# Kernel optimization log

Hardware: AMD Instinct MI355X
Metric: run time of the kernel (lower is better)

The kernel has to match this reference:

```python
import jax, jax.numpy as jnp
import numpy as np

B, T, C, HR = 8, 4096, 256, 4
N_LAYER, LAYER_ID = 12, 3
HID = HR * C


def _fancy_decay_first():
    # Faithful reproduction of VRWKV_SpatialMix._init_weights(init_mode='fancy')
    r01 = LAYER_ID / (N_LAYER - 1)
    h = np.arange(C, dtype=np.float32)
    decay = -5.0 + 8.0 * (h / (C - 1)) ** (0.7 + 1.3 * r01)
    zig = ((np.arange(1, C + 1) % 3) - 1).astype(np.float32) * 0.5
    first = np.float32(np.log(0.3)) + zig
    return jnp.asarray(decay, jnp.float32), jnp.asarray(first, jnp.float32)


def setup_inputs() -> dict:
    key = jax.random.key(0)
    ks = jax.random.split(key, 12)
    s = 0.02  # small weight scale keeps exp(k) well-conditioned
    decay, first = _fancy_decay_first()
    return {
        "x": jax.random.normal(ks[0], (B, T, C), jnp.float32),
        "Wk": jax.random.normal(ks[1], (C, C), jnp.float32) * s,
        "Wv": jax.random.normal(ks[2], (C, C), jnp.float32) * s,
        "Wr": jax.random.normal(ks[3], (C, C), jnp.float32) * s,
        "Wo": jax.random.normal(ks[4], (C, C), jnp.float32) * s,
        "Wk_ffn": jax.random.normal(ks[5], (C, HID), jnp.float32) * s,
        "Wv_ffn": jax.random.normal(ks[6], (HID, C), jnp.float32) * s,
        "Wr_ffn": jax.random.normal(ks[7], (C, C), jnp.float32) * s,
        "g1": 1.0 + 0.1 * jax.random.normal(ks[8], (C,), jnp.float32),
        "b1": 0.1 * jax.random.normal(ks[9], (C,), jnp.float32),
        "g2": 1.0 + 0.1 * jax.random.normal(ks[10], (C,), jnp.float32),
        "b2": 0.1 * jax.random.normal(ks[11], (C,), jnp.float32),
        "spatial_decay": decay,
        "spatial_first": first,
    }


def _ln(x, g, b):
    m = jnp.mean(x, axis=-1, keepdims=True)
    v = jnp.var(x, axis=-1, keepdims=True)
    return (x - m) * jax.lax.rsqrt(v + 1e-5) * g + b


def _wkv(w, u, k, v):
    # Numerically-stable log-space WKV recurrence (same math as wkv_cuda):
    # y_t = (sum_{i<t} e^{w*(t-1-i)+k_i} v_i + e^{u+k_t} v_t)
    #     / (sum_{i<t} e^{w*(t-1-i)+k_i}     + e^{u+k_t})
    # w,u: [C]; k,v: [B,T,C] -> y: [B,T,C]
    Bb, Tt, Cc = k.shape
    kT = jnp.swapaxes(k, 0, 1)  # [T,B,C]
    vT = jnp.swapaxes(v, 0, 1)

    def step(carry, kv):
        p, q, o = carry           # [B,C] num / den / running max exponent
        kt, vt = kv               # [B,C]
        no = jnp.maximum(o, u + kt)
        A = jnp.exp(o - no)
        E = jnp.exp(u + kt - no)
        y = (A * p + E * vt) / (A * q + E)
        no2 = jnp.maximum(w + o, kt)
        A2 = jnp.exp(w + o - no2)
        E2 = jnp.exp(kt - no2)
        return (A2 * p + E2 * vt, A2 * q + E2, no2), y

    init = (jnp.zeros((Bb, Cc), k.dtype),
            jnp.zeros((Bb, Cc), k.dtype),
            jnp.full((Bb, Cc), -1e38, k.dtype))
    _, yT = jax.lax.scan(step, init, (kT, vT))
    return jnp.swapaxes(yT, 0, 1)


def reference(x, Wk, Wv, Wr, Wo, Wk_ffn, Wv_ffn, Wr_ffn, g1, b1, g2, b2,
              spatial_decay, spatial_first):
    Tlen = x.shape[1]
    # --- SpatialMix (shift_pixel=0 -> xk=xv=xr=h, key_norm=False) ---
    h = _ln(x, g1, b1)
    k = h @ Wk
    v = h @ Wv
    sr = jax.nn.sigmoid(h @ Wr)
    y = _wkv(spatial_decay / Tlen, spatial_first / Tlen, k, v)
    x = x + (sr * y) @ Wo
    # --- ChannelMix (square-ReLU MLP, sigmoid receptance gate) ---
    h2 = _ln(x, g2, b2)
    kk = jnp.square(jax.nn.relu(h2 @ Wk_ffn))
    x = x + jax.nn.sigmoid(h2 @ Wr_ffn) * (kk @ Wv_ffn)
    return x
```

## Files before the change

kernel.cpp:

```cpp
#include <hip/hip_runtime.h>
#include <hip/hip_bf16.h>
#include <math.h>

#define TDIM 4096
#define CDIM 256
#define BDIM 8
#define NTOK (BDIM * TDIM)
#define HIDDIM 1024
#define NCHUNK 256
#define CHLEN 16
#define NSEG 8
#define SEGCH 32

typedef float f32x4 __attribute__((ext_vector_type(4)));
typedef __bf16 bf16x8 __attribute__((ext_vector_type(8)));
typedef __bf16 bf16x4 __attribute__((ext_vector_type(4)));
typedef long long i64x2 __attribute__((ext_vector_type(2)));

#define GLDS16(gp, lp) __builtin_amdgcn_global_load_lds( \
    (const __attribute__((address_space(1))) void*)(gp), \
    (__attribute__((address_space(3))) void*)(lp), 16, 0, 0)

#define WAITCNT_VM8  0x0F78
#define WAITCNT_VM5  0x0F75
#define WAITCNT_VM4  0x0F74
#define WAITCNT_VM2  0x0F72
#define WAITCNT_VM0  0x0F70
#define WAITCNT_LGKM0 0xC07F

#define STAGE_FENCE() do { \
    __builtin_amdgcn_sched_barrier(0); \
    __builtin_amdgcn_s_waitcnt(WAITCNT_LGKM0); \
    __builtin_amdgcn_s_barrier(); \
    __builtin_amdgcn_sched_barrier(0); \
  } while (0)

__device__ __forceinline__ float sigm(float v) { return 1.0f / (1.0f + __expf(-v)); }

__device__ __forceinline__ int permk(int k) {
  return (k & ~63) + (((k >> 3) & 3) << 4) + (((k >> 5) & 1) << 3) + (k & 7);
}

__global__ __launch_bounds__(256) void prep(
    const float* __restrict__ Wk, const float* __restrict__ Wv,
    const float* __restrict__ Wr, const float* __restrict__ Wo,
    const float* __restrict__ Wkf, const float* __restrict__ Wvf,
    const float* __restrict__ Wrf,
    __bf16* __restrict__ WoT, unsigned char* __restrict__ Wkvr8,
    unsigned char* __restrict__ Wkfr8, unsigned char* __restrict__ Wvf8,
    const float* __restrict__ x, const float* __restrict__ gamma,
    const float* __restrict__ beta, unsigned char* __restrict__ h8) {
  if (blockIdx.x >= 1024) {
    const int wave = threadIdx.x >> 6, lane = threadIdx.x & 63;
    const long long row = (long long)(blockIdx.x - 1024) * 4 + wave;
    const long long base = row * CDIM + lane * 4;
    const f32x4 v = *(const f32x4*)&x[base];
    float s = v[0] + v[1] + v[2] + v[3];
    float s2 = v[0]*v[0] + v[1]*v[1] + v[2]*v[2] + v[3]*v[3];
    #pragma unroll
    for (int o = 1; o < 64; o <<= 1) { s += __shfl_xor(s, o); s2 += __shfl_xor(s2, o); }
    const float mean = s * (1.0f / CDIM);
    const float var = s2 * (1.0f / CDIM) - mean * mean;
    const float rstd = rsqrtf(var + 1e-5f);
    const f32x4 g4 = *(const f32x4*)&gamma[lane * 4];
    const f32x4 b4 = *(const f32x4*)&beta[lane * 4];
    float o0 = (v[0] - mean) * rstd * g4[0] + b4[0];
    float o1 = (v[1] - mean) * rstd * g4[1] + b4[1];
    float o2 = (v[2] - mean) * rstd * g4[2] + b4[2];
    float o3 = (v[3] - mean) * rstd * g4[3] + b4[3];
    int w = 0;
    w = __builtin_amdgcn_cvt_pk_fp8_f32(o0, o1, w, false);
    w = __builtin_amdgcn_cvt_pk_fp8_f32(o2, o3, w, true);
    *(int*)&h8[row * CDIM + permk(lane * 4)] = w;
    return;
  }
  long long j = (long long)blockIdx.x * 256 + threadIdx.x;
  if (j < 49152) {
    const long long d = j * 4;
    const int n = (int)(d >> 8), k0 = (int)(d & 255);
    const float* src = (n < 256) ? Wk : (n < 512 ? Wv : Wr);
    const int nn = n & 255;
    int w = 0;
    w = __builtin_amdgcn_cvt_pk_fp8_f32(src[k0 * 256 + nn],
                                        src[(k0 + 1) * 256 + nn], w, false);
    w = __builtin_amdgcn_cvt_pk_fp8_f32(src[(k0 + 2) * 256 + nn],
                                        src[(k0 + 3) * 256 + nn], w, true);
    *(int*)&Wkvr8[(long long)n * 256 + permk(k0)] = w;
    return;
  }
  j -= 49152;
  if (j < 65536) { int n = (int)(j >> 8), k = (int)(j & 255);
    WoT[j] = (__bf16)Wo[k * 256 + n]; return; }
  j -= 65536;
  if (j < 81920) {
    const long long d = j * 4;
    const int n = (int)(d >> 8), k0 = (int)(d & 255);
    float v0, v1, v2, v3;
    if (n < 1024) {
      v0 = Wkf[(long long)k0 * 1024 + n];       v1 = Wkf[(long long)(k0 + 1) * 1024 + n];
      v2 = Wkf[(long long)(k0 + 2) * 1024 + n]; v3 = Wkf[(long long)(k0 + 3) * 1024 + n];
    } else {
      const int m = n - 1024;
      v0 = Wrf[k0 * 256 + m];       v1 = Wrf[(k0 + 1) * 256 + m];
      v2 = Wrf[(k0 + 2) * 256 + m]; v3 = Wrf[(k0 + 3) * 256 + m];
    }
    int w = 0;
    w = __builtin_amdgcn_cvt_pk_fp8_f32(v0, v1, w, false);
    w = __builtin_amdgcn_cvt_pk_fp8_f32(v2, v3, w, true);
    *(int*)&Wkfr8[(long long)n * 256 + permk(k0)] = w;
    return;
  }
  j -= 81920;
  if (j < 65536) {
    const long long d = j * 4;
    const int n = (int)(d >> 10), k0 = (int)(d & 1023);
    int w = 0;
    w = __builtin_amdgcn_cvt_pk_fp8_f32(Wvf[(long long)k0 * 256 + n],
                                        Wvf[(long long)(k0 + 1) * 256 + n], w, false);
    w = __builtin_amdgcn_cvt_pk_fp8_f32(Wvf[(long long)(k0 + 2) * 256 + n],
                                        Wvf[(long long)(k0 + 3) * 256 + n], w, true);
    *(int*)&Wvf8[(long long)n * 1024 + permk(k0)] = w;
    return;
  }
}

template <int EPI, int NY>
__global__ __launch_bounds__(512, 4) void gemmF(
    const unsigned char* __restrict__ A8, const unsigned char* __restrict__ B8,
    __bf16* __restrict__ outH, __bf16* __restrict__ outH2,
    unsigned char* __restrict__ outC) {
  constexpr int NTILES = 256 * NY;
  constexpr int TPB = NTILES / 512;
  static_assert(NTILES % 512 == 0, "grid divisibility");
  __shared__ unsigned char sA[2][4 * 8192];

  const int tid = threadIdx.x;
  const int wave = tid >> 6, lane = tid & 63;
  const int quad = lane >> 4, mrow = lane & 15;
  const int wm = (wave & 1) * 64, wn = (wave >> 1) * 32;
  const int srow = lane >> 2;
  const int o16 = (lane & 3) * 16;
  const int t0 = blockIdx.x * TPB;

  auto issueA = [&](int t, int buf) {
    const long long bm = (long long)(t & 255) * 128;
    const int r0 = wave * 16;
    #pragma unroll
    for (int g = 0; g < 4; g++)
      GLDS16(A8 + (bm + r0 + srow) * 256 + g * 64 + o16,
             &sA[buf][g * 8192 + r0 * 64]);
  };

  i64x2 fb[2][4];
  auto loadB = [&](int y) {
    const long long bn = (long long)y * 128;
    #pragma unroll
    for (int nt = 0; nt < 2; nt++)
      #pragma unroll
      for (int g = 0; g < 4; g++)
        fb[nt][g] = *(const i64x2*)
            &B8[(bn + wn + nt * 16 + mrow) * 256 + g * 64 + quad * 16];
  };

  issueA(t0, 0);
  int prevy = -1;

  #pragma unroll 1
  for (int i = 0; i < TPB; i++) {
    const int t = t0 + i;
    const int y = t >> 8;
    const bool ych = (y != prevy);
    prevy = y;

    if (i == 0)          __builtin_amdgcn_s_waitcnt(WAITCNT_VM0);
    else if (EPI == 0)   __builtin_amdgcn_s_waitcnt(WAITCNT_VM4);
    else                 __builtin_amdgcn_s_waitcnt(WAITCNT_VM2);
    __builtin_amdgcn_s_barrier();

    if (ych) loadB(y);
    if (i + 1 < TPB) issueA(t + 1, (i + 1) & 1);

    f32x4 acc[4][2] = {};
    const int buf = i & 1;
    #pragma unroll
    for (int g = 0; g < 4; g++) {
      i64x2 fa[4];
      #pragma unroll
      for (int mt = 0; mt < 4; mt++)
        fa[mt] = *(const i64x2*)
            &sA[buf][g * 8192 + (wm + mt * 16 + mrow) * 64 + quad * 16];
      #pragma unroll
      for (int c = 0; c < 2; c++)
        #pragma unroll
        for (int mt = 0; mt < 4; mt++)
          #pragma unroll
          for (int nt = 0; nt < 2; nt++)
            acc[mt][nt] = __builtin_amdgcn_mfma_f32_16x16x32_fp8_fp8(
                fb[nt][g][c], fa[mt][c], acc[mt][nt], 0, 0, 0);
    }

    __builtin_amdgcn_s_barrier();
    unsigned char* stg = &sA[buf][0];
    const long long bm = (long long)(t & 255) * 128;

    if (EPI == 0) {
      const int plane = y >> 1;
      #pragma unroll
      for (int mt = 0; mt < 4; mt++) {
        const int row = wm + mt * 16 + mrow;
        const int swz = (row & 7) << 4;
        #pragma unroll
        for (int nt = 0; nt < 2; nt++) {
          const f32x4 a = acc[mt][nt];
          bf16x4 v;
          if (plane == 2) {
            #pragma unroll
            for (int r = 0; r < 4; r++) v[r] = (__bf16)sigm(a[r]);
          } else {
            #pragma unroll
            for (int r = 0; r < 4; r++) v[r] = (__bf16)a[r];
          }
          const int cb2 = (wn + nt * 16 + quad * 4) * 2;
          *(bf16x4*)&stg[row * 256 + (cb2 ^ swz)] = v;
        }
      }
      STAGE_FENCE();
      char* ob = (char*)(outH + (long long)plane * (32768LL * 256));
      const int row = tid >> 2, qb = (tid & 3) * 64;
      const int swz = (row & 7) << 4;
      const long long gb = (bm + row) * 512 + (long long)(y & 1) * 256 + qb;
      #pragma unroll
      for (int c = 0; c < 4; c++) {
        const i64x2 d = *(const i64x2*)&stg[row * 256 + ((qb + c * 16) ^ swz)];
        *(i64x2*)&ob[gb + c * 16] = d;
      }
    } else {
      if (y < 8) {
        #pragma unroll
        for (int mt = 0; mt < 4; mt++) {
          const int row = wm + mt * 16 + mrow;
          const int swz = (row & 7) << 4;
          #pragma unroll
          for (int nt = 0; nt < 2; nt++) {
            const f32x4 a = acc[mt][nt];
            float q0 = a[0] > 0.0f ? a[0] : 0.0f;
            float q1 = a[1] > 0.0f ? a[1] : 0.0f;
            float q2 = a[2] > 0.0f ? a[2] : 0.0f;
            float q3 = a[3] > 0.0f ? a[3] : 0.0f;
            int w = 0;
            w = __builtin_amdgcn_cvt_pk_fp8_f32(q0 * q0, q1 * q1, w, false);
            w = __builtin_amdgcn_cvt_pk_fp8_f32(q2 * q2, q3 * q3, w, true);
            const int cbl = wn + nt * 16 + quad * 4;
            *(int*)&stg[row * 128 + (permk(cbl) ^ swz)] = w;
          }
        }
        STAGE_FENCE();
        const int row = tid >> 2, sb = (tid & 3) * 32;
        const int swz = (row & 7) << 4;
        const long long gb = (bm + row) * 1024 + (long long)y * 128 + sb;
        #pragma unroll
        for (int c = 0; c < 2; c++) {
          const i64x2 d = *(const i64x2*)&stg[row * 128 + ((sb + c * 16) ^ swz)];
          *(i64x2*)&outC[gb + c * 16] = d;
        }
      } else {
        #pragma unroll
        for (int mt = 0; mt < 4; mt++) {
          const int row = wm + mt * 16 + mrow;
          const int swz = (row & 7) << 4;
          #pragma unroll
          for (int nt = 0; nt < 2; nt++) {
            const f32x4 a = acc[mt][nt];
            bf16x4 v;
            #pragma unroll
            for (int r = 0; r < 4; r++) v[r] = (__bf16)sigm(a[r]);
            const int cb2 = (wn + nt * 16 + quad * 4) * 2;
            *(bf16x4*)&stg[row * 256 + (cb2 ^ swz)] = v;
          }
        }
        STAGE_FENCE();
        char* ob = (char*)outH2;
        const int row = tid >> 2, qb = (tid & 3) * 64;
        const int swz = (row & 7) << 4;
        const long long gb = (bm + row) * 512 + (long long)(y - 8) * 256 + qb;
        #pragma unroll
        for (int c = 0; c < 4; c++) {
          const i64x2 d = *(const i64x2*)&stg[row * 256 + ((qb + c * 16) ^ swz)];
          *(i64x2*)&ob[gb + c * 16] = d;
        }
      }
    }
  }
}

template <int K, int EPI>
__global__ __launch_bounds__(256, 3) void gemm9(
    const unsigned char* __restrict__ A8, const unsigned char* __restrict__ B8,
    int M, __bf16* __restrict__ outH, __bf16* __restrict__ outH2,
    unsigned char* __restrict__ outC,
    float* __restrict__ outF, const __bf16* __restrict__ srcH,
    const __bf16* __restrict__ gate) {
  constexpr int NIT = K / 64;
  __shared__ unsigned char sA[3][128 * 64];
  __shared__ unsigned char sB[3][128 * 64];
  const int tid = threadIdx.x;
  const int wave = tid >> 6, lane = tid & 63;
  const int quad = lane >> 4, mrow = lane & 15;
  const long long bm = (long long)blockIdx.x * 128;
  const long long bn = (long long)blockIdx.y * 128;
  const int wm = (wave & 1) * 64, wn = (wave >> 1) * 64;
  const int srow = lane >> 2;
  const int o16 = (lane & 3) * 16;

  auto issue = [&](int g) {
    const int buf = g % 3;
    const long long k0 = (long long)g * 64;
    const int a0 = wave * 32;
    GLDS16(A8 + (bm + a0 + srow) * (long long)K + k0 + o16, &sA[buf][a0 * 64]);
    GLDS16(A8 + (bm + a0 + 16 + srow) * (long long)K + k0 + o16, &sA[buf][(a0 + 16) * 64]);
    GLDS16(B8 + (bn + a0 + srow) * (long long)K + k0 + o16, &sB[buf][a0 * 64]);
    GLDS16(B8 + (bn + a0 + 16 + srow) * (long long)K + k0 + o16, &sB[buf][(a0 + 16) * 64]);
  };

  f32x4 acc[4][4] = {};
  issue(0);
  if (NIT > 1) issue(1);

  auto compute = [&](int g) {
    const int buf = g % 3;
    i64x2 fa[4], fb[4];
    #pragma unroll
    for (int mt = 0; mt < 4; mt++)
      fa[mt] = *(const i64x2*)&sA[buf][(wm + mt * 16 + mrow) * 64 + quad * 16];
    #pragma unroll
    for (int nt = 0; nt < 4; nt++)
      fb[nt] = *(const i64x2*)&sB[buf][(wn + nt * 16 + mrow) * 64 + quad * 16];
    #pragma unroll
    for (int c = 0; c < 2; c++)
      #pragma unroll
      for (int mt = 0; mt < 4; mt++)
        #pragma unroll
        for (int nt = 0; nt < 4; nt++)
          acc[mt][nt] = __builtin_amdgcn_mfma_f32_16x16x32_fp8_fp8(
              fb[nt][c], fa[mt][c], acc[mt][nt], 0, 0, 0);
  };

  #pragma unroll 1
  for (int g = 0; g < NIT; g++) {
    if (g == NIT - 1) {
      __builtin_amdgcn_s_waitcnt(WAITCNT_VM0);
    } else {
      __builtin_amdgcn_s_waitcnt(WAITCNT_VM4);
    }
    __builtin_amdgcn_s_barrier();
    if (g + 2 < NIT) issue(g + 2);
    compute(g);
  }

  #pragma unroll
  for (int mt = 0; mt < 4; mt++) {
    #pragma unroll
    for (int nt = 0; nt < 4; nt++) {
      const long long row = bm + wm + mt * 16 + mrow;
      const long long colb = bn + wn + nt * 16 + quad * 4;
      const f32x4 a = acc[mt][nt];
      const long long idx = row * 256 + colb;
      const bf16x4 s4 = *(const bf16x4*)&srcH[idx];
      const bf16x4 g4 = *(const bf16x4*)&gate[idx];
      f32x4 v;
      #pragma unroll
      for (int r = 0; r < 4; r++) v[r] = (float)s4[r] + (float)g4[r] * a[r];
      *(f32x4*)&outF[idx] = v;
    }
  }
}

__global__ __launch_bounds__(256, 2) void gemm7(
    const __bf16* __restrict__ A, const __bf16* __restrict__ Bt,
    const float* __restrict__ x,
    const float* __restrict__ gammaP, const float* __restrict__ betaP,
    __bf16* __restrict__ x1h, unsigned char* __restrict__ h28) {
  constexpr int K = 256;
  __shared__ __bf16 sA[3][64 * 32];
  __shared__ __bf16 sB[3][256 * 32];
  __shared__ float redS[4][64], redQ[4][64];

  const int tid = threadIdx.x;
  const int wave = tid >> 6, lane = tid & 63;
  const int quad = lane >> 4, mrow = lane & 15;
  const long long bm = (long long)blockIdx.x * 64;
  const int wn = wave * 64;
  const int lrow = lane >> 2;
  const int lk = (lane & 3) * 8;

  auto issue = [&](int g) {
    const int buf = g % 3;
    const long long k0 = (long long)g * 32;
    GLDS16(A + (bm + wave * 16 + lrow) * (long long)K + k0 + lk,
           &sA[buf][(wave * 16) * 32]);
    #pragma unroll
    for (int bc = 0; bc < 4; bc++) {
      const int r0 = wave * 64 + bc * 16;
      GLDS16(Bt + (r0 + lrow) * (long long)K + k0 + lk, &sB[buf][r0 * 32]);
    }
  };

  f32x4 acc[4][4] = {};

  auto compute = [&](int g) {
    const int buf = g % 3;
    bf16x8 fa[4], fb[4];
    #pragma unroll
    for (int mt = 0; mt < 4; mt++)
      fa[mt] = *(const bf16x8*)&sA[buf][(mt * 16 + mrow) * 32 + quad * 8];
    #pragma unroll
    for (int nt = 0; nt < 4; nt++)
      fb[nt] = *(const bf16x8*)&sB[buf][(wn + nt * 16 + mrow) * 32 + quad * 8];
    #pragma unroll
    for (int mt = 0; mt < 4; mt++)
      #pragma unroll
      for (int nt = 0; nt < 4; nt++)
        acc[mt][nt] = __builtin_amdgcn_mfma_f32_16x16x32_bf16(fb[nt], fa[mt], acc[mt][nt], 0, 0, 0);
  };

  issue(0);
  issue(1);
  #pragma unroll 1
  for (int g = 0; g < 8; g++) {
    if (g == 7) {
      __builtin_amdgcn_s_waitcnt(WAITCNT_VM0);
    } else {
      __builtin_amdgcn_s_waitcnt(WAITCNT_VM5);
    }
    __builtin_amdgcn_s_barrier();
    if (g + 2 < 8) issue(g + 2);
    compute(g);
  }

  float sum[4] = {0, 0, 0, 0}, sq[4] = {0, 0, 0, 0};
  #pragma unroll
  for (int mt = 0; mt < 4; mt++) {
    #pragma unroll
    for (int nt = 0; nt < 4; nt++) {
      const long long row = bm + mt * 16 + mrow;
      const long long colb = wn + nt * 16 + quad * 4;
      acc[mt][nt] += *(const f32x4*)&x[row * 256 + colb];
      #pragma unroll
      for (int r = 0; r < 4; r++) {
        sum[mt] += acc[mt][nt][r];
        sq[mt] += acc[mt][nt][r] * acc[mt][nt][r];
      }
    }
  }
  #pragma unroll
  for (int mt = 0; mt < 4; mt++) {
    sum[mt] += __shfl_xor(sum[mt], 16); sq[mt] += __shfl_xor(sq[mt], 16);
    sum[mt] += __shfl_xor(sum[mt], 32); sq[mt] += __shfl_xor(sq[mt], 32);
  }
  if (quad == 0) {
    #pragma unroll
    for (int mt = 0; mt < 4; mt++) {
      redS[wave][mt * 16 + mrow] = sum[mt];
      redQ[wave][mt * 16 + mrow] = sq[mt];
    }
  }
  __syncthreads();
  #pragma unroll
  for (int mt = 0; mt < 4; mt++) {
    const int rb = mt * 16 + mrow;
    const float ts = redS[0][rb] + redS[1][rb] + redS[2][rb] + redS[3][rb];
    const float tq = redQ[0][rb] + redQ[1][rb] + redQ[2][rb] + redQ[3][rb];
    const float mean = ts * (1.0f / 256.0f);
    const float rstd = rsqrtf(tq * (1.0f / 256.0f) - mean * mean + 1e-5f);
    const long long row = bm + rb;
    #pragma unroll
    for (int nt = 0; nt < 4; nt++) {
      const long long colb = wn + nt * 16 + quad * 4;
      const f32x4 g4 = *(const f32x4*)&gammaP[colb];
      const f32x4 b4 = *(const f32x4*)&betaP[colb];
      bf16x4 xo;
      const float t0 = acc[mt][nt][0], t1 = acc[mt][nt][1];
      const float t2 = acc[mt][nt][2], t3 = acc[mt][nt][3];
      xo[0] = (__bf16)t0; xo[1] = (__bf16)t1; xo[2] = (__bf16)t2; xo[3] = (__bf16)t3;
      const float h0 = (t0 - mean) * rstd * g4[0] + b4[0];
      const float h1 = (t1 - mean) * rstd * g4[1] + b4[1];
      const float h2v = (t2 - mean) * rstd * g4[2] + b4[2];
      const float h3 = (t3 - mean) * rstd * g4[3] + b4[3];
      *(bf16x4*)&x1h[row * 256 + colb] = xo;
      int w = 0;
      w = __builtin_amdgcn_cvt_pk_fp8_f32(h0, h1, w, false);
      w = __builtin_amdgcn_cvt_pk_fp8_f32(h2v, h3, w, true);
      *(int*)&h28[row * 256 + permk((int)colb)] = w;
    }
  }
}

__global__ __launch_bounds__(256) void wkv_phase1(
    const __bf16* __restrict__ ka, const __bf16* __restrict__ va,
    const float* __restrict__ decay,
    float* __restrict__ Sloc, float* __restrict__ Zloc) {
  const int wave = threadIdx.x >> 6, lane = threadIdx.x & 63;
  const int gi = blockIdx.x * 4 + wave;
  const int b = gi >> 8, chunk = gi & (NCHUNK - 1);
  const int c0 = lane * 4;
  const f32x4 w4 = *(const f32x4*)&decay[c0];
  f32x4 ew;
  #pragma unroll
  for (int r = 0; r < 4; r++) ew[r] = __expf(w4[r] * (1.0f / TDIM));
  f32x4 S = {0,0,0,0}, Z = {0,0,0,0};
  long long base = ((long long)b * TDIM + (long long)chunk * CHLEN) * 256 + c0;
  #pragma unroll 4
  for (int t = 0; t < CHLEN; t++) {
    const bf16x4 k4 = *(const bf16x4*)&ka[base + (long long)t * 256];
    const bf16x4 v4 = *(const bf16x4*)&va[base + (long long)t * 256];
    #pragma unroll
    for (int r = 0; r < 4; r++) {
      const float ek = __expf((float)k4[r]);
      S[r] = ew[r] * S[r] + ek * (float)v4[r];
      Z[r] = ew[r] * Z[r] + ek;
    }
  }
  const long long o = (long long)gi * 256 + c0;
  *(f32x4*)&Sloc[o] = S;
  *(f32x4*)&Zloc[o] = Z;
}

__global__ __launch_bounds__(256) void wkv_phase2a(
    const float* __restrict__ Sloc, const float* __restrict__ Zloc,
    const float* __restrict__ decay,
    float* __restrict__ LprefS, float* __restrict__ LprefZ,
    float* __restrict__ TS, float* __restrict__ TZ) {
  const int b = blockIdx.x >> 3, seg = blockIdx.x & 7;
  const int c = threadIdx.x;
  const float w = decay[c] * (1.0f / TDIM);
  const float ewL = __expf(w * (float)CHLEN);
  float S = 0.0f, Z = 0.0f;
  long long o = ((long long)(b * NCHUNK + seg * SEGCH)) * 256 + c;
  #pragma unroll 4
  for (int i = 0; i < SEGCH; i++, o += 256) {
    LprefS[o] = S;
    LprefZ[o] = Z;
    S = ewL * S + Sloc[o];
    Z = ewL * Z + Zloc[o];
  }
  const int to = (b * NSEG + seg) * 256 + c;
  TS[to] = S;
  TZ[to] = Z;
}

__global__ __launch_bounds__(256) void wkv_phase3(
    const __bf16* __restrict__ ka, const __bf16* __restrict__ va,
    const __bf16* __restrict__ ra,
    const float* __restrict__ decay, const float* __restrict__ first,
    const float* __restrict__ LprefS, const float* __restrict__ LprefZ,
    const float* __restrict__ TS, const float* __restrict__ TZ,
    __bf16* __restrict__ a2) {
  const int wave = threadIdx.x >> 6, lane = threadIdx.x & 63;
  const int gi = blockIdx.x * 4 + wave;
  const int b = gi >> 8, chunk = gi & (NCHUNK - 1);
  const int seg = chunk >> 5, d = chunk & (SEGCH - 1);
  const int c0 = lane * 4;
  const f32x4 w4 = *(const f32x4*)&decay[c0];
  const f32x4 u4 = *(const f32x4*)&first[c0];
  f32x4 ew, eu;
  #pragma unroll
  for (int r = 0; r < 4; r++) {
    ew[r] = __expf(w4[r] * (1.0f / TDIM));
    eu[r] = __expf(u4[r] * (1.0f / TDIM));
  }
  const long long so = (long long)gi * 256 + c0;
  const f32x4 Lp = *(const f32x4*)&LprefS[so];
  const f32x4 LpZ = *(const f32x4*)&LprefZ[so];
  f32x4 S, Z;
  #pragma unroll
  for (int r = 0; r < 4; r++) {
    const float wr = w4[r] * (1.0f / TDIM);
    const float ew32 = __expf(wr * (float)(CHLEN * SEGCH));
    float CS = 0.0f, CZ = 0.0f;
    const int tb = b * NSEG * 256 + c0 + r;
    for (int s = 0; s < seg; s++) {
      CS = ew32 * CS + TS[tb + s * 256];
      CZ = ew32 * CZ + TZ[tb + s * 256];
    }
    const float f0 = __expf(wr * (float)(CHLEN * d));
    S[r] = f0 * CS + Lp[r];
    Z[r] = f0 * CZ + LpZ[r];
  }
  long long base = ((long long)b * TDIM + (long long)chunk * CHLEN) * 256 + c0;
  #pragma unroll 2
  for (int t = 0; t < CHLEN; t++) {
    const long long p = base + (long long)t * 256;
    const bf16x4 k4 = *(const bf16x4*)&ka[p];
    const bf16x4 v4 = *(const bf16x4*)&va[p];
    const bf16x4 r4 = *(const bf16x4*)&ra[p];
    bf16x4 o;
    #pragma unroll
    for (int r = 0; r < 4; r++) {
      const float ek = __expf((float)k4[r]);
      const float E = eu[r] * ek;
      const float y = (S[r] + E * (float)v4[r]) / (Z[r] + E);
      o[r] = (__bf16)((float)r4[r] * y);
      S[r] = ew[r] * S[r] + ek * (float)v4[r];
      Z[r] = ew[r] * Z[r] + ek;
    }
    *(bf16x4*)&a2[p] = o;
  }
}

extern "C" void kernel_launch(void* const* d_in, const int* in_sizes, int n_in,
                              void* d_out, int out_size, void* d_ws, size_t ws_size,
                              hipStream_t stream) {
  const float* x     = (const float*)d_in[0];
  const float* Wk    = (const float*)d_in[1];
  const float* Wv    = (const float*)d_in[2];
  const float* Wr    = (const float*)d_in[3];
  const float* Wo    = (const float*)d_in[4];
  const float* Wkf   = (const float*)d_in[5];
  const float* Wvf   = (const float*)d_in[6];
  const float* Wrf   = (const float*)d_in[7];
  const float* g1    = (const float*)d_in[8];
  const float* b1    = (const float*)d_in[9];
  const float* g2    = (const float*)d_in[10];
  const float* b2    = (const float*)d_in[11];
  const float* decay = (const float*)d_in[12];
  const float* first = (const float*)d_in[13];
  float* out = (float*)d_out;
  char* ws = (char*)d_ws;

  __bf16* ka     = (__bf16*)(ws + 0);
  __bf16* va     = (__bf16*)(ws + 16777216LL);
  __bf16* ra     = (__bf16*)(ws + 33554432LL);
  __bf16* a2     = (__bf16*)(ws + 50331648LL);
  __bf16* g2buf  = (__bf16*)(ws + 50331648LL);
  unsigned char* h8  = (unsigned char*)(ws + 67108864LL);
  unsigned char* h28 = (unsigned char*)(ws + 67108864LL);
  __bf16* x1h    = (__bf16*)(ws + 83886080LL);
  unsigned char* kk8 = (unsigned char*)(ws + 100663296LL);
  float*  Sloc   = (float*)(ws + 134217728LL);
  float*  Zloc   = (float*)(ws + 137363456LL);
  float*  LprefS = (float*)(ws + 140509184LL);
  float*  LprefZ = (float*)(ws + 143654912LL);
  float*  TS     = (float*)(ws + 146800640LL);
  float*  TZ     = (float*)(ws + 146866176LL);
  __bf16* WoT    = (__bf16*)(ws + 167772160LL);
  unsigned char* Wkvr8 = (unsigned char*)(ws + 167903232LL);
  unsigned char* Wkfr8 = (unsigned char*)(ws + 168099840LL);
  unsigned char* Wvf8  = (unsigned char*)(ws + 168427520LL);

  prep<<<1024 + NTOK / 4, 256, 0, stream>>>(
      Wk, Wv, Wr, Wo, Wkf, Wvf, Wrf, WoT, Wkvr8, Wkfr8, Wvf8,
      x, g1, b1, h8);

  gemmF<0, 6><<<512, 512, 0, stream>>>(h8, Wkvr8, ka, nullptr, nullptr);
  wkv_phase1<<<BDIM * NCHUNK / 4, 256, 0, stream>>>(ka, va, decay, Sloc, Zloc);
  wkv_phase2a<<<BDIM * NSEG, 256, 0, stream>>>(Sloc, Zloc, decay,
                                               LprefS, LprefZ, TS, TZ);
  wkv_phase3<<<BDIM * NCHUNK / 4, 256, 0, stream>>>(ka, va, ra, decay, first,
                                                    LprefS, LprefZ, TS, TZ, a2);
  gemm7<<<NTOK / 64, 256, 0, stream>>>(a2, WoT, x, g2, b2, x1h, h28);

  gemmF<2, 10><<<512, 512, 0, stream>>>(h28, Wkfr8, nullptr, g2buf, kk8);
  gemm9<1024, 3><<<dim3(NTOK / 128, 2), 256, 0, stream>>>(
      kk8, Wvf8, NTOK, nullptr, nullptr, nullptr, out, x1h, g2buf);
}
```

Baseline: 252.6 us.

## Fuse WKV phase-3 recurrence into output-projection GEMM via shared-memory A tile

Merges the WKV phase-3 scan kernel with the following Wo projection + residual + LayerNorm GEMM. Each block computes the gated WKV output for its 64 tokens (4 chunks of 16) and writes it straight into LDS in K-sliced layout, where the GEMM consumes it. This removes the a2 round trip through global memory and one kernel launch. In exchange the B pipeline drops from triple to double buffering with a full vmcnt(0) wait each step, and the scan's latency is no longer hidden behind other blocks' GEMM work inside a separate kernel.

After: 247.9 us. About the same (-1.9%).

```diff
diff --git a/kernel.cpp b/kernel.cpp
--- a/kernel.cpp
+++ b/kernel.cpp
@@ -375,126 +375,6 @@
   }
 }
 
-__global__ __launch_bounds__(256, 2) void gemm7(
-    const __bf16* __restrict__ A, const __bf16* __restrict__ Bt,
-    const float* __restrict__ x,
-    const float* __restrict__ gammaP, const float* __restrict__ betaP,
-    __bf16* __restrict__ x1h, unsigned char* __restrict__ h28) {
-  constexpr int K = 256;
-  __shared__ __bf16 sA[3][64 * 32];
-  __shared__ __bf16 sB[3][256 * 32];
-  __shared__ float redS[4][64], redQ[4][64];
-
-  const int tid = threadIdx.x;
-  const int wave = tid >> 6, lane = tid & 63;
-  const int quad = lane >> 4, mrow = lane & 15;
-  const long long bm = (long long)blockIdx.x * 64;
-  const int wn = wave * 64;
-  const int lrow = lane >> 2;
-  const int lk = (lane & 3) * 8;
-
-  auto issue = [&](int g) {
-    const int buf = g % 3;
-    const long long k0 = (long long)g * 32;
-    GLDS16(A + (bm + wave * 16 + lrow) * (long long)K + k0 + lk,
-           &sA[buf][(wave * 16) * 32]);
-    #pragma unroll
-    for (int bc = 0; bc < 4; bc++) {
-      const int r0 = wave * 64 + bc * 16;
-      GLDS16(Bt + (r0 + lrow) * (long long)K + k0 + lk, &sB[buf][r0 * 32]);
-    }
-  };
-
-  f32x4 acc[4][4] = {};
-
-  auto compute = [&](int g) {
-    const int buf = g % 3;
-    bf16x8 fa[4], fb[4];
-    #pragma unroll
-    for (int mt = 0; mt < 4; mt++)
-      fa[mt] = *(const bf16x8*)&sA[buf][(mt * 16 + mrow) * 32 + quad * 8];
-    #pragma unroll
-    for (int nt = 0; nt < 4; nt++)
-      fb[nt] = *(const bf16x8*)&sB[buf][(wn + nt * 16 + mrow) * 32 + quad * 8];
-    #pragma unroll
-    for (int mt = 0; mt < 4; mt++)
-      #pragma unroll
-      for (int nt = 0; nt < 4; nt++)
-        acc[mt][nt] = __builtin_amdgcn_mfma_f32_16x16x32_bf16(fb[nt], fa[mt], acc[mt][nt], 0, 0, 0);
-  };
-
-  issue(0);
-  issue(1);
-  #pragma unroll 1
-  for (int g = 0; g < 8; g++) {
-    if (g == 7) {
-      __builtin_amdgcn_s_waitcnt(WAITCNT_VM0);
-    } else {
-      __builtin_amdgcn_s_waitcnt(WAITCNT_VM5);
-    }
-    __builtin_amdgcn_s_barrier();
-    if (g + 2 < 8) issue(g + 2);
-    compute(g);
-  }
-
-  float sum[4] = {0, 0, 0, 0}, sq[4] = {0, 0, 0, 0};
-  #pragma unroll
-  for (int mt = 0; mt < 4; mt++) {
-    #pragma unroll
-    for (int nt = 0; nt < 4; nt++) {
-      const long long row = bm + mt * 16 + mrow;
-      const long long colb = wn + nt * 16 + quad * 4;
-      acc[mt][nt] += *(const f32x4*)&x[row * 256 + colb];
-      #pragma unroll
-      for (int r = 0; r < 4; r++) {
-        sum[mt] += acc[mt][nt][r];
-        sq[mt] += acc[mt][nt][r] * acc[mt][nt][r];
-      }
-    }
-  }
-  #pragma unroll
-  for (int mt = 0; mt < 4; mt++) {
-    sum[mt] += __shfl_xor(sum[mt], 16); sq[mt] += __shfl_xor(sq[mt], 16);
-    sum[mt] += __shfl_xor(sum[mt], 32); sq[mt] += __shfl_xor(sq[mt], 32);
-  }
-  if (quad == 0) {
-    #pragma unroll
-    for (int mt = 0; mt < 4; mt++) {
-      redS[wave][mt * 16 + mrow] = sum[mt];
-      redQ[wave][mt * 16 + mrow] = sq[mt];
-    }
-  }
-  __syncthreads();
-  #pragma unroll
-  for (int mt = 0; mt < 4; mt++) {
-    const int rb = mt * 16 + mrow;
-    const float ts = redS[0][rb] + redS[1][rb] + redS[2][rb] + redS[3][rb];
-    const float tq = redQ[0][rb] + redQ[1][rb] + redQ[2][rb] + redQ[3][rb];
-    const float mean = ts * (1.0f / 256.0f);
-    const float rstd = rsqrtf(tq * (1.0f / 256.0f) - mean * mean + 1e-5f);
-    const long long row = bm + rb;
-    #pragma unroll
-    for (int nt = 0; nt < 4; nt++) {
-      const long long colb = wn + nt * 16 + quad * 4;
-      const f32x4 g4 = *(const f32x4*)&gammaP[colb];
-      const f32x4 b4 = *(const f32x4*)&betaP[colb];
-      bf16x4 xo;
-      const float t0 = acc[mt][nt][0], t1 = acc[mt][nt][1];
-      const float t2 = acc[mt][nt][2], t3 = acc[mt][nt][3];
-      xo[0] = (__bf16)t0; xo[1] = (__bf16)t1; xo[2] = (__bf16)t2; xo[3] = (__bf16)t3;
-      const float h0 = (t0 - mean) * rstd * g4[0] + b4[0];
-      const float h1 = (t1 - mean) * rstd * g4[1] + b4[1];
-      const float h2v = (t2 - mean) * rstd * g4[2] + b4[2];
-      const float h3 = (t3 - mean) * rstd * g4[3] + b4[3];
-      *(bf16x4*)&x1h[row * 256 + colb] = xo;
-      int w = 0;
-      w = __builtin_amdgcn_cvt_pk_fp8_f32(h0, h1, w, false);
-      w = __builtin_amdgcn_cvt_pk_fp8_f32(h2v, h3, w, true);
-      *(int*)&h28[row * 256 + permk((int)colb)] = w;
-    }
-  }
-}
-
 __global__ __launch_bounds__(256) void wkv_phase1(
     const __bf16* __restrict__ ka, const __bf16* __restrict__ va,
     const float* __restrict__ decay,
@@ -548,62 +428,174 @@
   TZ[to] = Z;
 }
 
-__global__ __launch_bounds__(256) void wkv_phase3(
+__global__ __launch_bounds__(256, 2) void wkv3_gemm7(
     const __bf16* __restrict__ ka, const __bf16* __restrict__ va,
     const __bf16* __restrict__ ra,
     const float* __restrict__ decay, const float* __restrict__ first,
     const float* __restrict__ LprefS, const float* __restrict__ LprefZ,
     const float* __restrict__ TS, const float* __restrict__ TZ,
-    __bf16* __restrict__ a2) {
-  const int wave = threadIdx.x >> 6, lane = threadIdx.x & 63;
-  const int gi = blockIdx.x * 4 + wave;
-  const int b = gi >> 8, chunk = gi & (NCHUNK - 1);
-  const int seg = chunk >> 5, d = chunk & (SEGCH - 1);
-  const int c0 = lane * 4;
-  const f32x4 w4 = *(const f32x4*)&decay[c0];
-  const f32x4 u4 = *(const f32x4*)&first[c0];
-  f32x4 ew, eu;
+    const __bf16* __restrict__ Bt,
+    const float* __restrict__ x,
+    const float* __restrict__ gammaP, const float* __restrict__ betaP,
+    __bf16* __restrict__ x1h, unsigned char* __restrict__ h28) {
+  __shared__ __bf16 sA2[8 * 64 * 32];
+  __shared__ __bf16 sB[2][256 * 32];
+  __shared__ float redS[4][64], redQ[4][64];
+
+  const int tid = threadIdx.x;
+  const int wave = tid >> 6, lane = tid & 63;
+  const int quad = lane >> 4, mrow = lane & 15;
+  const long long bm = (long long)blockIdx.x * 64;
+  const int wn = wave * 64;
+  const int lrow = lane >> 2;
+  const int lk = (lane & 3) * 8;
+
+  auto issue = [&](int g) {
+    const int buf = g & 1;
+    const long long k0 = (long long)g * 32;
+    #pragma unroll
+    for (int bc = 0; bc < 4; bc++) {
+      const int r0 = wave * 64 + bc * 16;
+      GLDS16(Bt + (r0 + lrow) * 256 + k0 + lk, &sB[buf][r0 * 32]);
+    }
+  };
+  issue(0);
+
+  {
+    const int gi = blockIdx.x * 4 + wave;
+    const int b = gi >> 8, chunk = gi & (NCHUNK - 1);
+    const int seg = chunk >> 5, d = chunk & (SEGCH - 1);
+    const int c0 = lane * 4;
+    const f32x4 w4 = *(const f32x4*)&decay[c0];
+    const f32x4 u4 = *(const f32x4*)&first[c0];
+    f32x4 ew, eu;
+    #pragma unroll
+    for (int r = 0; r < 4; r++) {
+      ew[r] = __expf(w4[r] * (1.0f / TDIM));
+      eu[r] = __expf(u4[r] * (1.0f / TDIM));
+    }
+    const long long so = (long long)gi * 256 + c0;
+    const f32x4 Lp = *(const f32x4*)&LprefS[so];
+    const f32x4 LpZ = *(const f32x4*)&LprefZ[so];
+    f32x4 S, Z;
+    #pragma unroll
+    for (int r = 0; r < 4; r++) {
+      const float wr = w4[r] * (1.0f / TDIM);
+      const float ew32 = __expf(wr * (float)(CHLEN * SEGCH));
+      float CS = 0.0f, CZ = 0.0f;
+      const int tb = b * NSEG * 256 + c0 + r;
+      for (int s = 0; s < seg; s++) {
+        CS = ew32 * CS + TS[tb + s * 256];
+        CZ = ew32 * CZ + TZ[tb + s * 256];
+      }
+      const float f0 = __expf(wr * (float)(CHLEN * d));
+      S[r] = f0 * CS + Lp[r];
+      Z[r] = f0 * CZ + LpZ[r];
+    }
+    long long gbase = ((long long)b * TDIM + (long long)chunk * CHLEN) * 256 + c0;
+    __bf16* arow = &sA2[(lane >> 3) * 2048 + (wave * 16) * 32 + (lane & 7) * 4];
+    #pragma unroll 2
+    for (int t = 0; t < CHLEN; t++) {
+      const long long p = gbase + (long long)t * 256;
+      const bf16x4 k4 = *(const bf16x4*)&ka[p];
+      const bf16x4 v4 = *(const bf16x4*)&va[p];
+      const bf16x4 r4 = *(const bf16x4*)&ra[p];
+      bf16x4 o;
+      #pragma unroll
+      for (int r = 0; r < 4; r++) {
+        const float ek = __expf((float)k4[r]);
+        const float E = eu[r] * ek;
+        const float y = (S[r] + E * (float)v4[r]) / (Z[r] + E);
+        o[r] = (__bf16)((float)r4[r] * y);
+        S[r] = ew[r] * S[r] + ek * (float)v4[r];
+        Z[r] = ew[r] * Z[r] + ek;
+      }
+      *(bf16x4*)&arow[t * 32] = o;
+    }
+  }
+  __syncthreads();
+
+  f32x4 acc[4][4] = {};
+
+  auto compute = [&](int g) {
+    const int buf = g & 1;
+    bf16x8 fa[4], fb[4];
+    #pragma unroll
+    for (int mt = 0; mt < 4; mt++)
+      fa[mt] = *(const bf16x8*)&sA2[g * 2048 + (mt * 16 + mrow) * 32 + quad * 8];
+    #pragma unroll
+    for (int nt = 0; nt < 4; nt++)
+      fb[nt] = *(const bf16x8*)&sB[buf][(wn + nt * 16 + mrow) * 32 + quad * 8];
+    #pragma unroll
+    for (int mt = 0; mt < 4; mt++)
+      #pragma unroll
+      for (int nt = 0; nt < 4; nt++)
+        acc[mt][nt] = __builtin_amdgcn_mfma_f32_16x16x32_bf16(fb[nt], fa[mt], acc[mt][nt], 0, 0, 0);
+  };
+
+  #pragma unroll 1
+  for (int g = 0; g < 8; g++) {
+    __builtin_amdgcn_s_waitcnt(WAITCNT_VM0);
+    __builtin_amdgcn_s_barrier();
+    if (g + 1 < 8) issue(g + 1);
+    compute(g);
+  }
+
+  float sum[4] = {0, 0, 0, 0}, sq[4] = {0, 0, 0, 0};
   #pragma unroll
-  for (int r = 0; r < 4; r++) {
-    ew[r] = __expf(w4[r] * (1.0f / TDIM));
-    eu[r] = __expf(u4[r] * (1.0f / TDIM));
-  }
-  const long long so = (long long)gi * 256 + c0;
-  const f32x4 Lp = *(const f32x4*)&LprefS[so];
-  const f32x4 LpZ = *(const f32x4*)&LprefZ[so];
-  f32x4 S, Z;
+  for (int mt = 0; mt < 4; mt++) {
+    #pragma unroll
+    for (int nt = 0; nt < 4; nt++) {
+      const long long row = bm + mt * 16 + mrow;
+      const long long colb = wn + nt * 16 + quad * 4;
+      acc[mt][nt] += *(const f32x4*)&x[row * 256 + colb];
+      #pragma unroll
+      for (int r = 0; r < 4; r++) {
+        sum[mt] += acc[mt][nt][r];
+        sq[mt] += acc[mt][nt][r] * acc[mt][nt][r];
+      }
+    }
+  }
   #pragma unroll
-  for (int r = 0; r < 4; r++) {
-    const float wr = w4[r] * (1.0f / TDIM);
-    const float ew32 = __expf(wr * (float)(CHLEN * SEGCH));
-    float CS = 0.0f, CZ = 0.0f;
-    const int tb = b * NSEG * 256 + c0 + r;
-    for (int s = 0; s < seg; s++) {
-      CS = ew32 * CS + TS[tb + s * 256];
-      CZ = ew32 * CZ + TZ[tb + s * 256];
-    }
-    const float f0 = __expf(wr * (float)(CHLEN * d));
-    S[r] = f0 * CS + Lp[r];
-    Z[r] = f0 * CZ + LpZ[r];
-  }
-  long long base = ((long long)b * TDIM + (long long)chunk * CHLEN) * 256 + c0;
-  #pragma unroll 2
-  for (int t = 0; t < CHLEN; t++) {
-    const long long p = base + (long long)t * 256;
-    const bf16x4 k4 = *(const bf16x4*)&ka[p];
-    const bf16x4 v4 = *(const bf16x4*)&va[p];
-    const bf16x4 r4 = *(const bf16x4*)&ra[p];
-    bf16x4 o;
-    #pragma unroll
-    for (int r = 0; r < 4; r++) {
-      const float ek = __expf((float)k4[r]);
-      const float E = eu[r] * ek;
-      const float y = (S[r] + E * (float)v4[r]) / (Z[r] + E);
-      o[r] = (__bf16)((float)r4[r] * y);
-      S[r] = ew[r] * S[r] + ek * (float)v4[r];
-      Z[r] = ew[r] * Z[r] + ek;
-    }
-    *(bf16x4*)&a2[p] = o;
+  for (int mt = 0; mt < 4; mt++) {
+    sum[mt] += __shfl_xor(sum[mt], 16); sq[mt] += __shfl_xor(sq[mt], 16);
+    sum[mt] += __shfl_xor(sum[mt], 32); sq[mt] += __shfl_xor(sq[mt], 32);
+  }
+  if (quad == 0) {
+    #pragma unroll
+    for (int mt = 0; mt < 4; mt++) {
+      redS[wave][mt * 16 + mrow] = sum[mt];
+      redQ[wave][mt * 16 + mrow] = sq[mt];
+    }
+  }
+  __syncthreads();
+  #pragma unroll
+  for (int mt = 0; mt < 4; mt++) {
+    const int rb = mt * 16 + mrow;
+    const float ts = redS[0][rb] + redS[1][rb] + redS[2][rb] + redS[3][rb];
+    const float tq = redQ[0][rb] + redQ[1][rb] + redQ[2][rb] + redQ[3][rb];
+    const float mean = ts * (1.0f / 256.0f);
+    const float rstd = rsqrtf(tq * (1.0f / 256.0f) - mean * mean + 1e-5f);
+    const long long row = bm + rb;
+    #pragma unroll
+    for (int nt = 0; nt < 4; nt++) {
+      const long long colb = wn + nt * 16 + quad * 4;
+      const f32x4 g4 = *(const f32x4*)&gammaP[colb];
+      const f32x4 b4 = *(const f32x4*)&betaP[colb];
+      bf16x4 xo;
+      const float t0 = acc[mt][nt][0], t1 = acc[mt][nt][1];
+      const float t2 = acc[mt][nt][2], t3 = acc[mt][nt][3];
+      xo[0] = (__bf16)t0; xo[1] = (__bf16)t1; xo[2] = (__bf16)t2; xo[3] = (__bf16)t3;
+      const float h0 = (t0 - mean) * rstd * g4[0] + b4[0];
+      const float h1 = (t1 - mean) * rstd * g4[1] + b4[1];
+      const float h2v = (t2 - mean) * rstd * g4[2] + b4[2];
+      const float h3 = (t3 - mean) * rstd * g4[3] + b4[3];
+      *(bf16x4*)&x1h[row * 256 + colb] = xo;
+      int w = 0;
+      w = __builtin_amdgcn_cvt_pk_fp8_f32(h0, h1, w, false);
+      w = __builtin_amdgcn_cvt_pk_fp8_f32(h2v, h3, w, true);
+      *(int*)&h28[row * 256 + permk((int)colb)] = w;
+    }
   }
 }
 
@@ -630,7 +622,6 @@
   __bf16* ka     = (__bf16*)(ws + 0);
   __bf16* va     = (__bf16*)(ws + 16777216LL);
   __bf16* ra     = (__bf16*)(ws + 33554432LL);
-  __bf16* a2     = (__bf16*)(ws + 50331648LL);
   __bf16* g2buf  = (__bf16*)(ws + 50331648LL);
   unsigned char* h8  = (unsigned char*)(ws + 67108864LL);
   unsigned char* h28 = (unsigned char*)(ws + 67108864LL);
@@ -655,9 +646,9 @@
   wkv_phase1<<<BDIM * NCHUNK / 4, 256, 0, stream>>>(ka, va, decay, Sloc, Zloc);
   wkv_phase2a<<<BDIM * NSEG, 256, 0, stream>>>(Sloc, Zloc, decay,
                                                LprefS, LprefZ, TS, TZ);
-  wkv_phase3<<<BDIM * NCHUNK / 4, 256, 0, stream>>>(ka, va, ra, decay, first,
-                                                    LprefS, LprefZ, TS, TZ, a2);
-  gemm7<<<NTOK / 64, 256, 0, stream>>>(a2, WoT, x, g2, b2, x1h, h28);
+  wkv3_gemm7<<<NTOK / 64, 256, 0, stream>>>(ka, va, ra, decay, first,
+                                            LprefS, LprefZ, TS, TZ,
+                                            WoT, x, g2, b2, x1h, h28);
 
   gemmF<2, 10><<<512, 512, 0, stream>>>(h28, Wkfr8, nullptr, g2buf, kk8);
   gemm9<1024, 3><<<dim3(NTOK / 128, 2), 256, 0, stream>>>(
```
